# Performance work log

Hardware: AMD Instinct MI355X
Metric: run time of the kernel (lower is better)

Reference implementation:

```python
import jax, jax.numpy as jnp
import numpy as np

P = 512        # n_predicates
C = 65536      # n_constants
L = 1          # max_rule_length (only runnable config of original code)


def setup_inputs() -> dict:
    key = jax.random.key(0)
    k1, k2 = jax.random.split(key)
    initial_facts = jax.random.uniform(k1, (P, C), dtype=jnp.float32)
    rule_weights = jax.random.normal(k2, (P, L, P), dtype=jnp.float32)
    return {"initial_facts": initial_facts, "rule_weights": rule_weights, "n_iterations": 3}


def reference(initial_facts, rule_weights, n_iterations):
    # F.softmax(rule[step], dim=0) on the 1-D vector rule_weights[r, 0, :]
    # == softmax over the last axis of rule_weights[:, 0, :].
    # Stacking apply_rule over all rules r is exactly A @ facts.
    A = jax.nn.softmax(rule_weights[:, 0, :], axis=-1)  # [P, P]
    facts = initial_facts                                # [P, C]
    for _ in range(n_iterations):
        derived = A @ facts                              # [P, C] (rule r -> row r)
        facts = jnp.maximum(facts, derived.max(axis=0))  # broadcast [C] over [P, C]
    return facts
```

## Files before the change

### kernel.cpp

```cpp
#include <hip/hip_runtime.h>
#include <hip/hip_bf16.h>
#include <cstdint>


typedef __attribute__((ext_vector_type(8))) short bf16x8;
typedef __attribute__((ext_vector_type(8))) unsigned short u16x8;
typedef __attribute__((ext_vector_type(16))) float f32x16;
typedef unsigned short ushort_t;
typedef unsigned int uint32;

#define PDIM 512
#define CDIM 65536
#define NT   64
#define WAVES 8

__device__ __forceinline__ ushort_t f2bf(float x) {
    uint32 u = __float_as_uint(x);
    return (ushort_t)((u + 0x7fffu + ((u >> 16) & 1u)) >> 16);
}
__device__ __forceinline__ float bf2f(uint32 bits) { return __uint_as_float(bits << 16); }

__device__ __forceinline__ bf16x8 pkmax8(bf16x8 v, ushort_t mu) {
    u16x8 a = __builtin_bit_cast(u16x8, v);
    const u16x8 mb = {mu, mu, mu, mu, mu, mu, mu, mu};
    a = __builtin_elementwise_max(a, mb);
    return __builtin_bit_cast(bf16x8, a);
}

__global__ __launch_bounds__(64) void softmax_pack(const float* __restrict__ rw,
                                                   ushort_t* __restrict__ Apk) {
    const int r  = blockIdx.x;
    const int ln = threadIdx.x;
    const float* row = rw + r * PDIM;
    float4 x0 = *(const float4*)(row + ln * 8);
    float4 x1 = *(const float4*)(row + ln * 8 + 4);
    float v[8] = {x0.x, x0.y, x0.z, x0.w, x1.x, x1.y, x1.z, x1.w};

    float mx = -1e30f;
    #pragma unroll
    for (int i = 0; i < 8; ++i) mx = fmaxf(mx, v[i]);
    #pragma unroll
    for (int d = 1; d < 64; d <<= 1) mx = fmaxf(mx, __shfl_xor(mx, d, 64));
    float s = 0.f;
    #pragma unroll
    for (int i = 0; i < 8; ++i) { v[i] = __expf(v[i] - mx); s += v[i]; }
    #pragma unroll
    for (int d = 1; d < 64; d <<= 1) s += __shfl_xor(s, d, 64);
    const float inv = 1.f / s;

    ushort_t o[8];
    #pragma unroll
    for (int i = 0; i < 8; ++i) o[i] = f2bf(v[i] * inv);
    const int idx16 = ((ln >> 1) * 16 + (r >> 5)) * 64 + ((ln & 1) << 5) + (r & 31);
    *(int4*)(Apk + idx16 * 8) = *(const int4*)o;
}

__global__ __launch_bounds__(512, 4) void ilp_kernel(
        const float* __restrict__ facts,
        const ushort_t* __restrict__ Apk,
        const int* __restrict__ n_iter_p,
        float* __restrict__ out) {
    __shared__ ushort_t ft[64 * NT * 8];
    __shared__ float wred[2][WAVES][NT];
    __shared__ float mfin[NT];

    const int tid  = threadIdx.x;
    const int wave = tid >> 6;
    const int lane = tid & 63;
    const int l31  = lane & 31;
    const int half = lane >> 5;
    const int c0   = blockIdx.x * NT;

    int n_iter = *n_iter_p;
    n_iter = n_iter < 0 ? 0 : (n_iter > 8 ? 8 : n_iter);

    {
        const int c = tid & 63;
        #pragma unroll 2
        for (int s = 0; s < 8; ++s) {
            const int g = wave * 8 + s;
            ushort_t gb[8];
            #pragma unroll
            for (int i = 0; i < 8; ++i)
                gb[i] = f2bf(facts[(g * 8 + i) * CDIM + c0 + c]);
            *(int4*)(&ft[(g * 64 + c) * 8]) = *(const int4*)gb;
        }
    }

    const ushort_t* abase = Apk + (wave * 128 + half * 32 + l31) * 8;
    bf16x8 aF[2][2], bR[2][2];
    aF[0][0] = *(const bf16x8*)(abase);
    aF[0][1] = *(const bf16x8*)(abase + 512);
    aF[1][0] = *(const bf16x8*)(abase + 8192);
    aF[1][1] = *(const bf16x8*)(abase + 8192 + 512);

    __syncthreads();

    const int bbase = (half * 64 + l31) * 8;
    bR[0][0] = *(const bf16x8*)(&ft[bbase]);
    bR[0][1] = *(const bf16x8*)(&ft[bbase + 256]);
    bR[1][0] = *(const bf16x8*)(&ft[bbase + 1024]);
    bR[1][1] = *(const bf16x8*)(&ft[bbase + 1024 + 256]);

    ushort_t ml[2] = {0, 0};
    float    mf[2] = {0.f, 0.f};

    #pragma unroll 1
    for (int it = 0; it < n_iter; ++it) {
        f32x16 acc[2][2];
        #pragma unroll
        for (int rt2 = 0; rt2 < 2; ++rt2)
            #pragma unroll
            for (int ct2 = 0; ct2 < 2; ++ct2)
                #pragma unroll
                for (int e = 0; e < 16; ++e) acc[rt2][ct2][e] = 0.f;

        #pragma unroll 2
        for (int kt2 = 0; kt2 < 32; ++kt2) {
            const int cur = kt2 & 1;
            const int ktp = (kt2 + 2) & 31;

            bf16x8 bC[2];
            bC[0] = pkmax8(bR[cur][0], ml[0]);
            bC[1] = pkmax8(bR[cur][1], ml[1]);

            __builtin_amdgcn_s_setprio(1);
            acc[0][0] = __builtin_amdgcn_mfma_f32_32x32x16_bf16(
                aF[cur][0], bC[0], acc[0][0], 0, 0, 0);
            acc[1][0] = __builtin_amdgcn_mfma_f32_32x32x16_bf16(
                aF[cur][1], bC[0], acc[1][0], 0, 0, 0);
            acc[0][1] = __builtin_amdgcn_mfma_f32_32x32x16_bf16(
                aF[cur][0], bC[1], acc[0][1], 0, 0, 0);
            acc[1][1] = __builtin_amdgcn_mfma_f32_32x32x16_bf16(
                aF[cur][1], bC[1], acc[1][1], 0, 0, 0);
            __builtin_amdgcn_s_setprio(0);

            {
                const ushort_t* ap = abase + ktp * 8192;
                aF[cur][0] = *(const bf16x8*)(ap);
                aF[cur][1] = *(const bf16x8*)(ap + 512);
                const int bo = bbase + ktp * 1024;
                bR[cur][0] = *(const bf16x8*)(&ft[bo]);
                bR[cur][1] = *(const bf16x8*)(&ft[bo + 256]);
            }
        }

        float mx[2];
        #pragma unroll
        for (int ct2 = 0; ct2 < 2; ++ct2) {
            float m0 = -1e30f;
            #pragma unroll
            for (int rt2 = 0; rt2 < 2; ++rt2)
                #pragma unroll
                for (int e = 0; e < 16; ++e) m0 = fmaxf(m0, acc[rt2][ct2][e]);
            m0 = fmaxf(m0, __shfl_xor(m0, 32, 64));
            mx[ct2] = m0;
        }
        const int buf = it & 1;
        if (half == 0) {
            #pragma unroll
            for (int ct2 = 0; ct2 < 2; ++ct2) wred[buf][wave][ct2 * 32 + l31] = mx[ct2];
        }
        __syncthreads();
        #pragma unroll
        for (int ct2 = 0; ct2 < 2; ++ct2) {
            const int c = ct2 * 32 + l31;
            float m = wred[buf][0][c];
            #pragma unroll
            for (int w = 1; w < WAVES; ++w) m = fmaxf(m, wred[buf][w][c]);
            mf[ct2] = fmaxf(mf[ct2], m);
            ml[ct2] = f2bf(mf[ct2]);
        }
    }

    if (wave == 0 && half == 0) {
        mfin[l31]      = mf[0];
        mfin[32 + l31] = mf[1];
    }
    __syncthreads();

    {
        const int c = tid & 63;
        const float m = mfin[c];
        #pragma unroll 2
        for (int s = 0; s < 8; ++s) {
            const int g = wave * 8 + s;
            ushort_t gb[8];
            *(int4*)gb = *(const int4*)(&ft[(g * 64 + c) * 8]);
            #pragma unroll
            for (int i = 0; i < 8; ++i)
                out[(g * 8 + i) * CDIM + c0 + c] = fmaxf(bf2f(gb[i]), m);
        }
    }
}

extern "C" void kernel_launch(void* const* d_in, const int* in_sizes, int n_in,
                              void* d_out, int out_size, void* d_ws, size_t ws_size,
                              hipStream_t stream) {
    const float* facts    = (const float*)d_in[0];
    const float* rw       = (const float*)d_in[1];
    const int*   n_iter_p = (const int*)d_in[2];
    float* out = (float*)d_out;

    ushort_t* Apk = (ushort_t*)d_ws;

    softmax_pack<<<PDIM, 64, 0, stream>>>(rw, Apk);
    ilp_kernel<<<CDIM / NT, 512, 0, stream>>>(facts, Apk, n_iter_p, out);
}
```

Before: 308.7 us.

## Apply running max to shared facts tile between iterations, vectorize global I/O

Instead of applying the per-column running max to the B operand inside the MFMA inner loop on every k-step, the kernel now updates the bf16 facts tile in shared memory once per iteration and reloads the B registers. This takes the packed max off the MFMA critical path. The cost is an extra shared-memory read-modify-write pass and an additional barrier per iteration. Global loads and stores also move from scalar floats to float2 so each thread handles two columns, which makes memory transactions wider. The final max is read from the last iteration's wave reductions.

```diff
diff --git a/kernel.cpp b/kernel.cpp
--- a/kernel.cpp
+++ b/kernel.cpp
@@ -61,8 +61,7 @@
         const int* __restrict__ n_iter_p,
         float* __restrict__ out) {
     __shared__ ushort_t ft[64 * NT * 8];
-    __shared__ float wred[2][WAVES][NT];
-    __shared__ float mfin[NT];
+    __shared__ float wred[WAVES][NT];
 
     const int tid  = threadIdx.x;
     const int wave = tid >> 6;
@@ -74,20 +73,27 @@
     int n_iter = *n_iter_p;
     n_iter = n_iter < 0 ? 0 : (n_iter > 8 ? 8 : n_iter);
 
+    wred[wave][lane] = 0.f;
+
     {
-        const int c = tid & 63;
+        const int c2  = (tid & 31) * 2;
+        const int grp = tid >> 5;
         #pragma unroll 2
-        for (int s = 0; s < 8; ++s) {
-            const int g = wave * 8 + s;
-            ushort_t gb[8];
-            #pragma unroll
-            for (int i = 0; i < 8; ++i)
-                gb[i] = f2bf(facts[(g * 8 + i) * CDIM + c0 + c]);
-            *(int4*)(&ft[(g * 64 + c) * 8]) = *(const int4*)gb;
+        for (int s = 0; s < 4; ++s) {
+            const int g = grp * 4 + s;
+            ushort_t ga[8], gb[8];
+            #pragma unroll
+            for (int i = 0; i < 8; ++i) {
+                const float2 v = *(const float2*)(facts + (g * 8 + i) * CDIM + c0 + c2);
+                ga[i] = f2bf(v.x);
+                gb[i] = f2bf(v.y);
+            }
+            *(int4*)(&ft[(g * NT + c2) * 8])     = *(const int4*)ga;
+            *(int4*)(&ft[(g * NT + c2 + 1) * 8]) = *(const int4*)gb;
         }
     }
 
-    const ushort_t* abase = Apk + (wave * 128 + half * 32 + l31) * 8;
+    const ushort_t* abase = Apk + wave * 1024 + (half * 32 + l31) * 8;
     bf16x8 aF[2][2], bR[2][2];
     aF[0][0] = *(const bf16x8*)(abase);
     aF[0][1] = *(const bf16x8*)(abase + 512);
@@ -96,14 +102,11 @@
 
     __syncthreads();
 
-    const int bbase = (half * 64 + l31) * 8;
+    const int bbase = (half * NT + l31) * 8;
     bR[0][0] = *(const bf16x8*)(&ft[bbase]);
     bR[0][1] = *(const bf16x8*)(&ft[bbase + 256]);
     bR[1][0] = *(const bf16x8*)(&ft[bbase + 1024]);
     bR[1][1] = *(const bf16x8*)(&ft[bbase + 1024 + 256]);
-
-    ushort_t ml[2] = {0, 0};
-    float    mf[2] = {0.f, 0.f};
 
     #pragma unroll 1
     for (int it = 0; it < n_iter; ++it) {
@@ -118,34 +121,27 @@
         #pragma unroll 2
         for (int kt2 = 0; kt2 < 32; ++kt2) {
             const int cur = kt2 & 1;
-            const int ktp = (kt2 + 2) & 31;
-
-            bf16x8 bC[2];
-            bC[0] = pkmax8(bR[cur][0], ml[0]);
-            bC[1] = pkmax8(bR[cur][1], ml[1]);
 
             __builtin_amdgcn_s_setprio(1);
             acc[0][0] = __builtin_amdgcn_mfma_f32_32x32x16_bf16(
-                aF[cur][0], bC[0], acc[0][0], 0, 0, 0);
+                aF[cur][0], bR[cur][0], acc[0][0], 0, 0, 0);
             acc[1][0] = __builtin_amdgcn_mfma_f32_32x32x16_bf16(
-                aF[cur][1], bC[0], acc[1][0], 0, 0, 0);
+                aF[cur][1], bR[cur][0], acc[1][0], 0, 0, 0);
             acc[0][1] = __builtin_amdgcn_mfma_f32_32x32x16_bf16(
-                aF[cur][0], bC[1], acc[0][1], 0, 0, 0);
+                aF[cur][0], bR[cur][1], acc[0][1], 0, 0, 0);
             acc[1][1] = __builtin_amdgcn_mfma_f32_32x32x16_bf16(
-                aF[cur][1], bC[1], acc[1][1], 0, 0, 0);
+                aF[cur][1], bR[cur][1], acc[1][1], 0, 0, 0);
             __builtin_amdgcn_s_setprio(0);
 
-            {
-                const ushort_t* ap = abase + ktp * 8192;
-                aF[cur][0] = *(const bf16x8*)(ap);
-                aF[cur][1] = *(const bf16x8*)(ap + 512);
-                const int bo = bbase + ktp * 1024;
-                bR[cur][0] = *(const bf16x8*)(&ft[bo]);
-                bR[cur][1] = *(const bf16x8*)(&ft[bo + 256]);
-            }
-        }
-
-        float mx[2];
+            const int ktp = (kt2 + 2) & 31;
+            const ushort_t* ap = abase + ktp * 8192;
+            aF[cur][0] = *(const bf16x8*)(ap);
+            aF[cur][1] = *(const bf16x8*)(ap + 512);
+            const int bo = bbase + ktp * 1024;
+            bR[cur][0] = *(const bf16x8*)(&ft[bo]);
+            bR[cur][1] = *(const bf16x8*)(&ft[bo + 256]);
+        }
+
         #pragma unroll
         for (int ct2 = 0; ct2 < 2; ++ct2) {
             float m0 = -1e30f;
@@ -154,42 +150,52 @@
                 #pragma unroll
                 for (int e = 0; e < 16; ++e) m0 = fmaxf(m0, acc[rt2][ct2][e]);
             m0 = fmaxf(m0, __shfl_xor(m0, 32, 64));
-            mx[ct2] = m0;
-        }
-        const int buf = it & 1;
-        if (half == 0) {
-            #pragma unroll
-            for (int ct2 = 0; ct2 < 2; ++ct2) wred[buf][wave][ct2 * 32 + l31] = mx[ct2];
+            if (half == 0) wred[wave][ct2 * 32 + l31] = m0;
         }
         __syncthreads();
+
+        if (it < n_iter - 1) {
+            const int c = tid & 63;
+            float m = wred[0][c];
+            #pragma unroll
+            for (int w = 1; w < WAVES; ++w) m = fmaxf(m, wred[w][c]);
+            const ushort_t mu = f2bf(m);
+            #pragma unroll
+            for (int s = 0; s < 8; ++s) {
+                const int idx = ((wave * 8 + s) * NT + c) * 8;
+                bf16x8 v = *(const bf16x8*)(&ft[idx]);
+                *(bf16x8*)(&ft[idx]) = pkmax8(v, mu);
+            }
+            __syncthreads();
+            bR[0][0] = *(const bf16x8*)(&ft[bbase]);
+            bR[0][1] = *(const bf16x8*)(&ft[bbase + 256]);
+            bR[1][0] = *(const bf16x8*)(&ft[bbase + 1024]);
+            bR[1][1] = *(const bf16x8*)(&ft[bbase + 1024 + 256]);
+        }
+    }
+
+    {
+        const int c2  = (tid & 31) * 2;
+        const int grp = tid >> 5;
+        float m0 = wred[0][c2], m1 = wred[0][c2 + 1];
         #pragma unroll
-        for (int ct2 = 0; ct2 < 2; ++ct2) {
-            const int c = ct2 * 32 + l31;
-            float m = wred[buf][0][c];
-            #pragma unroll
-            for (int w = 1; w < WAVES; ++w) m = fmaxf(m, wred[buf][w][c]);
-            mf[ct2] = fmaxf(mf[ct2], m);
-            ml[ct2] = f2bf(mf[ct2]);
-        }
-    }
-
-    if (wave == 0 && half == 0) {
-        mfin[l31]      = mf[0];
-        mfin[32 + l31] = mf[1];
-    }
-    __syncthreads();
-
-    {
-        const int c = tid & 63;
-        const float m = mfin[c];
+        for (int w = 1; w < WAVES; ++w) {
+            m0 = fmaxf(m0, wred[w][c2]);
+            m1 = fmaxf(m1, wred[w][c2 + 1]);
+        }
         #pragma unroll 2
-        for (int s = 0; s < 8; ++s) {
-            const int g = wave * 8 + s;
-            ushort_t gb[8];
-            *(int4*)gb = *(const int4*)(&ft[(g * 64 + c) * 8]);
-            #pragma unroll
-            for (int i = 0; i < 8; ++i)
-                out[(g * 8 + i) * CDIM + c0 + c] = fmaxf(bf2f(gb[i]), m);
+        for (int s = 0; s < 4; ++s) {
+            const int g = grp * 4 + s;
+            ushort_t ga[8], gb[8];
+            *(int4*)ga = *(const int4*)(&ft[(g * NT + c2) * 8]);
+            *(int4*)gb = *(const int4*)(&ft[(g * NT + c2 + 1) * 8]);
+            #pragma unroll
+            for (int i = 0; i < 8; ++i) {
+                float2 v;
+                v.x = fmaxf(bf2f(ga[i]), m0);
+                v.y = fmaxf(bf2f(gb[i]), m1);
+                *(float2*)(out + (g * 8 + i) * CDIM + c0 + c2) = v;
+            }
         }
     }
 }
```

New measurement: 309.5 us. About the same (+0.2%).
